# Performance work log

Measured on AMD Instinct MI355X. Metric: run time of the kernel, lower is better.

Reference implementation:

```python
import jax, jax.numpy as jnp
import numpy as np

B = 8192
I = 1024
H = 1024


def _xavier(key, out_dim, in_dim):
    limit = float(np.sqrt(6.0 / (in_dim + out_dim)))
    return jax.random.uniform(key, (out_dim, in_dim), jnp.float32, -limit, limit)


def setup_inputs() -> dict:
    key = jax.random.key(0)
    ks = jax.random.split(key, 16)
    inp = {
        "x": jax.random.normal(ks[0], (B, I), jnp.float32),
        "h_prev": jax.random.normal(ks[1], (B, H), jnp.float32),
        "c_prev": jax.random.normal(ks[2], (B, H), jnp.float32),
        # input->hidden weights (hidden_size, input_size), hidden->hidden (hidden_size, hidden_size)
        "Wxi": _xavier(ks[3], H, I), "Whi": _xavier(ks[4], H, H),
        "Wxf": _xavier(ks[5], H, I), "Whf": _xavier(ks[6], H, H),
        "Wxc": _xavier(ks[7], H, I), "Whc": _xavier(ks[8], H, H),
        "Wxo": _xavier(ks[9], H, I), "Who": _xavier(ks[10], H, H),
        "bxi": jnp.zeros((H,), jnp.float32), "bhi": jnp.zeros((H,), jnp.float32),
        # forget-gate biases initialized to ones per _init_weights
        "bxf": jnp.ones((H,), jnp.float32), "bhf": jnp.ones((H,), jnp.float32),
        "bxc": jnp.zeros((H,), jnp.float32), "bhc": jnp.zeros((H,), jnp.float32),
        "bxo": jnp.zeros((H,), jnp.float32), "bho": jnp.zeros((H,), jnp.float32),
    }
    return inp


def reference(x, h_prev, c_prev,
              Wxi, Whi, Wxf, Whf, Wxc, Whc, Wxo, Who,
              bxi, bhi, bxf, bhf, bxc, bhc, bxo, bho):
    # Fuse the 8 small linears into two GEMMs: stack along the output (gate) axis.
    Wx = jnp.concatenate([Wxi, Wxf, Wxc, Wxo], axis=0)   # (4H, I)
    Wh = jnp.concatenate([Whi, Whf, Whc, Who], axis=0)   # (4H, H)
    bx = jnp.concatenate([bxi, bxf, bxc, bxo], axis=0)    # (4H,)
    bh = jnp.concatenate([bhi, bhf, bhc, bho], axis=0)    # (4H,)
    gates = x @ Wx.T + h_prev @ Wh.T + (bx + bh)           # (B, 4H)
    zi, zf, zc, zo = jnp.split(gates, 4, axis=1)
    i = jax.nn.sigmoid(zi)
    f = jax.nn.sigmoid(zf)
    g = jnp.tanh(zc)
    o = jax.nn.sigmoid(zo)
    c_new = f * c_prev + i * g
    h_new = o * jnp.tanh(c_new)
    return (h_new, c_new)
```

## Files before the change

### kernel.cpp

```cpp
#include <hip/hip_runtime.h>
#include <hip/hip_bf16.h>
#include <stdint.h>


#define B_DIM 8192
#define I_DIM 1024
#define H_DIM 1024
#define K_DIM 2048
#define N_DIM 4096
#define NKT   32

typedef short bf16x8 __attribute__((ext_vector_type(8)));
typedef float f32x4 __attribute__((ext_vector_type(4)));

__device__ __forceinline__ unsigned short f2bf(float f) {
  unsigned int u = __float_as_uint(f);
  u += 0x7FFFu + ((u >> 16) & 1u);
  return (unsigned short)(u >> 16);
}

__global__ void pack_AB_kernel(const float* __restrict__ x, const float* __restrict__ h,
                               const float* __restrict__ Wxi, const float* __restrict__ Whi,
                               const float* __restrict__ Wxf, const float* __restrict__ Whf,
                               const float* __restrict__ Wxc, const float* __restrict__ Whc,
                               const float* __restrict__ Wxo, const float* __restrict__ Who,
                               unsigned short* __restrict__ outA,
                               unsigned short* __restrict__ outB) {
  const int totalA = B_DIM * K_DIM / 8;
  const int total  = totalA + N_DIM * K_DIM / 8;
  for (int idx = blockIdx.x * blockDim.x + threadIdx.x; idx < total;
       idx += gridDim.x * blockDim.x) {
    const float* src;
    unsigned short* dst;
    if (idx < totalA) {
      int row = idx >> 8;
      int col = (idx & 255) * 8;
      src = (col < I_DIM) ? (x + (size_t)row * I_DIM + col)
                          : (h + (size_t)row * H_DIM + (col - I_DIM));
      dst = outA + (size_t)idx * 8;
    } else {
      int u2 = idx - totalA;
      int lane_ = u2 & 63, nn = (u2 >> 6) & 3, kk = (u2 >> 8) & 1;
      int kt = (u2 >> 9) & 31, wn = (u2 >> 14) & 3, bn = u2 >> 16;
      int r = bn * 256 + wn * 64 + nn * 16 + (lane_ & 15);
      int k = kt * 64 + kk * 32 + (lane_ >> 4) * 8;
      int g = (r >> 4) & 3;
      int hh = ((r >> 6) << 4) | (r & 15);
      src = (k < I_DIM)
          ? ((g == 0 ? Wxi : g == 1 ? Wxf : g == 2 ? Wxc : Wxo) + (size_t)hh * I_DIM + k)
          : ((g == 0 ? Whi : g == 1 ? Whf : g == 2 ? Whc : Who) + (size_t)hh * H_DIM + (k - I_DIM));
      dst = outB + (size_t)u2 * 8;
    }
    const float4* s4 = (const float4*)src;
    float4 v0 = s4[0], v1 = s4[1];
    bf16x8 o;
    o[0] = f2bf(v0.x); o[1] = f2bf(v0.y); o[2] = f2bf(v0.z); o[3] = f2bf(v0.w);
    o[4] = f2bf(v1.x); o[5] = f2bf(v1.y); o[6] = f2bf(v1.z); o[7] = f2bf(v1.w);
    *(bf16x8*)dst = o;
  }
}


#define QUAD(MH, KOFF, BR) do {                                               \
    bf16x8 aq[4];                                                             \
    _Pragma("unroll") for (int mf = 0; mf < 4; ++mf)                          \
      aq[mf] = *(const bf16x8*)(ldsAr + _bo + (MH)*8192 + mf * 2048 + (KOFF));\
    __builtin_amdgcn_s_setprio(1);                                            \
    _Pragma("unroll") for (int mf = 0; mf < 4; ++mf)                          \
    _Pragma("unroll") for (int nn = 0; nn < 4; ++nn)                          \
      acc[(MH)*4 + mf][nn] = __builtin_amdgcn_mfma_f32_16x16x32_bf16(         \
          aq[mf], BR[nn], acc[(MH)*4 + mf][nn], 0, 0, 0);                     \
    __builtin_amdgcn_s_setprio(0);                                            \
  } while (0)

#define KTILE(BUF, KT, BC0, BN0) do {                                         \
    const int _bo  = (BUF) * 32768;                                           \
    const int _bo1 = ((BUF) ^ 1) * 32768;                                     \
    int _kt1 = (KT) + 1 < NKT ? (KT) + 1 : NKT - 1;                           \
    const unsigned short* _ga = gAst + (size_t)_kt1 * 64;                     \
    bf16x8 ar0 = *(const bf16x8*)(_ga);                                       \
    bf16x8 ar1 = *(const bf16x8*)(_ga + 8);                                   \
    bf16x8 ar2 = *(const bf16x8*)(_ga + 16);                                  \
    bf16x8 ar3 = *(const bf16x8*)(_ga + 24);                                  \
    _Pragma("unroll") for (int nn = 0; nn < 4; ++nn)                          \
      Bk1[nn] = *(const bf16x8*)(gBfr + (size_t)(KT) * 4096 + 2048 + nn*512); \
    _Pragma("unroll") for (int nn = 0; nn < 4; ++nn)                          \
      BN0[nn] = *(const bf16x8*)(gBfr + (size_t)_kt1 * 4096 + nn * 512);      \
    QUAD(0, rd0, BC0);                                                        \
    QUAD(1, rd0, BC0);                                                        \
    *(bf16x8*)(ldsAw + _bo1 + woff0) = ar0;                                   \
    *(bf16x8*)(ldsAw + _bo1 + woff1) = ar1;                                   \
    QUAD(0, rd1, Bk1);                                                        \
    QUAD(1, rd1, Bk1);                                                        \
    *(bf16x8*)(ldsAw + _bo1 + woff2) = ar2;                                   \
    *(bf16x8*)(ldsAw + _bo1 + woff3) = ar3;                                   \
    __syncthreads();                                                          \
  } while (0)

__launch_bounds__(512, 2)
__global__ void lstm_gemm_kernel(const unsigned short* __restrict__ A,
                                 const unsigned short* __restrict__ Bp,
                                 const float* __restrict__ c_prev,
                                 const float* __restrict__ bxi, const float* __restrict__ bhi,
                                 const float* __restrict__ bxf, const float* __restrict__ bhf,
                                 const float* __restrict__ bxc, const float* __restrict__ bhc,
                                 const float* __restrict__ bxo, const float* __restrict__ bho,
                                 float* __restrict__ out) {
  __shared__ __align__(16) char lds[65536];

  const int nwg = gridDim.x;
  int bid = blockIdx.x;
  int q = nwg >> 3;
  int wg = (bid & 7) * q + (bid >> 3);
  int bm = wg >> 4;
  int bn = wg & 15;

  int tid = threadIdx.x;
  int lane = tid & 63;
  int wid = tid >> 6;
  int wm = wid >> 2;
  int wn = wid & 3;

  const unsigned short* gAst = A + (size_t)(bm * 256 + (tid >> 1)) * K_DIM + (tid & 1) * 32;
  char* ldsAw = lds + (tid >> 1) * 128;
  int wr7 = (tid >> 1) & 7;
  int woff0 = ((((tid & 1) * 4 + 0) ^ wr7) << 4);
  int woff1 = ((((tid & 1) * 4 + 1) ^ wr7) << 4);
  int woff2 = ((((tid & 1) * 4 + 2) ^ wr7) << 4);
  int woff3 = ((((tid & 1) * 4 + 3) ^ wr7) << 4);

  const unsigned short* gBfr = Bp + (size_t)(bn * 4 + wn) * 131072 + lane * 8;

  int c15 = lane & 15;
  int kl = lane >> 4;
  const char* ldsAr = lds + wm * 16384 + c15 * 128;
  int rd0 = ((kl) ^ (lane & 7)) << 4;
  int rd1 = ((4 | kl) ^ (lane & 7)) << 4;

  f32x4 acc[8][4];
  f32x4 zero = {0.f, 0.f, 0.f, 0.f};
#pragma unroll
  for (int m = 0; m < 8; ++m)
#pragma unroll
    for (int n = 0; n < 4; ++n) acc[m][n] = zero;

  bf16x8 Bk0A[4], Bk0B[4], Bk1[4];

#pragma unroll
  for (int nn = 0; nn < 4; ++nn)
    Bk0A[nn] = *(const bf16x8*)(gBfr + nn * 512);
  {
    bf16x8 a0 = *(const bf16x8*)(gAst);
    bf16x8 a1 = *(const bf16x8*)(gAst + 8);
    bf16x8 a2 = *(const bf16x8*)(gAst + 16);
    bf16x8 a3 = *(const bf16x8*)(gAst + 24);
    *(bf16x8*)(ldsAw + woff0) = a0;
    *(bf16x8*)(ldsAw + woff1) = a1;
    *(bf16x8*)(ldsAw + woff2) = a2;
    *(bf16x8*)(ldsAw + woff3) = a3;
  }
  __syncthreads();

#pragma unroll 1
  for (int kt = 0; kt < NKT; kt += 2) {
    KTILE(0, kt, Bk0A, Bk0B);
    KTILE(1, kt + 1, Bk0B, Bk0A);
  }

  int h = (bn * 4 + wn) * 16 + c15;
  float bi = bxi[h] + bhi[h];
  float bf_ = bxf[h] + bhf[h];
  float bc = bxc[h] + bhc[h];
  float bo = bxo[h] + bho[h];
  int row0 = bm * 256 + wm * 128 + kl * 4;
#pragma unroll
  for (int mi = 0; mi < 8; ++mi) {
#pragma unroll
    for (int j = 0; j < 4; ++j) {
      int r = row0 + mi * 16 + j;
      size_t off = (size_t)r * H_DIM + h;
      float zi = acc[mi][0][j] + bi;
      float zf = acc[mi][1][j] + bf_;
      float zc = acc[mi][2][j] + bc;
      float zo = acc[mi][3][j] + bo;
      float ig = 1.f / (1.f + __expf(-zi));
      float fg = 1.f / (1.f + __expf(-zf));
      float e2 = __expf(-2.f * zc);
      float gg = (1.f - e2) / (1.f + e2);
      float og = 1.f / (1.f + __expf(-zo));
      float cp = c_prev[off];
      float cn = fg * cp + ig * gg;
      float e2c = __expf(-2.f * cn);
      float th = (1.f - e2c) / (1.f + e2c);
      out[off] = og * th;
      out[(size_t)B_DIM * H_DIM + off] = cn;
    }
  }
}

extern "C" void kernel_launch(void* const* d_in, const int* in_sizes, int n_in,
                              void* d_out, int out_size, void* d_ws, size_t ws_size,
                              hipStream_t stream) {
  const float* x      = (const float*)d_in[0];
  const float* h_prev = (const float*)d_in[1];
  const float* c_prev = (const float*)d_in[2];
  const float* Wxi = (const float*)d_in[3];
  const float* Whi = (const float*)d_in[4];
  const float* Wxf = (const float*)d_in[5];
  const float* Whf = (const float*)d_in[6];
  const float* Wxc = (const float*)d_in[7];
  const float* Whc = (const float*)d_in[8];
  const float* Wxo = (const float*)d_in[9];
  const float* Who = (const float*)d_in[10];
  const float* bxi = (const float*)d_in[11];
  const float* bhi = (const float*)d_in[12];
  const float* bxf = (const float*)d_in[13];
  const float* bhf = (const float*)d_in[14];
  const float* bxc = (const float*)d_in[15];
  const float* bhc = (const float*)d_in[16];
  const float* bxo = (const float*)d_in[17];
  const float* bho = (const float*)d_in[18];

  unsigned short* Abf = (unsigned short*)d_ws;
  unsigned short* Bbf = (unsigned short*)((char*)d_ws + (size_t)B_DIM * K_DIM * 2);

  pack_AB_kernel<<<2048, 256, 0, stream>>>(x, h_prev,
      Wxi, Whi, Wxf, Whf, Wxc, Whc, Wxo, Who, Abf, Bbf);
  lstm_gemm_kernel<<<512, 512, 0, stream>>>(Abf, Bbf, c_prev,
      bxi, bhi, bxf, bhf, bxc, bhc, bxo, bho, (float*)d_out);
}
```

Measured before the change: 163.8 us.

## Convert activations to bf16 inside GEMM and stage weights via direct-to-LDS loads

Drops the separate pass that packed x and h_prev into bf16 in a workspace. The GEMM now reads fp32 activations directly and converts them while writing to LDS. Weights are packed row-major and staged into LDS with global_load_lds async copies, double-buffered, instead of being read from a fragment-packed layout straight into registers. This removes an extra round trip to global memory for the activation matrix. In exchange, LDS per block doubles to 128KB, which likely breaks the two-blocks-per-CU launch bound, and each block reads twice as many activation bytes.

```diff
diff --git a/kernel.cpp b/kernel.cpp
--- a/kernel.cpp
+++ b/kernel.cpp
@@ -19,47 +19,60 @@
   return (unsigned short)(u >> 16);
 }
 
-__global__ void pack_AB_kernel(const float* __restrict__ x, const float* __restrict__ h,
-                               const float* __restrict__ Wxi, const float* __restrict__ Whi,
-                               const float* __restrict__ Wxf, const float* __restrict__ Whf,
-                               const float* __restrict__ Wxc, const float* __restrict__ Whc,
-                               const float* __restrict__ Wxo, const float* __restrict__ Who,
-                               unsigned short* __restrict__ outA,
-                               unsigned short* __restrict__ outB) {
-  const int totalA = B_DIM * K_DIM / 8;
-  const int total  = totalA + N_DIM * K_DIM / 8;
+__device__ __forceinline__ short f2bf16s(float f) {
+  __hip_bfloat16 t = __float2bfloat16(f);
+  return *reinterpret_cast<short*>(&t);
+}
+
+__device__ __forceinline__ bf16x8 cvt8(float4 a, float4 b) {
+  bf16x8 o;
+  o[0] = f2bf16s(a.x); o[1] = f2bf16s(a.y); o[2] = f2bf16s(a.z); o[3] = f2bf16s(a.w);
+  o[4] = f2bf16s(b.x); o[5] = f2bf16s(b.y); o[6] = f2bf16s(b.z); o[7] = f2bf16s(b.w);
+  return o;
+}
+
+__global__ void pack_B_kernel(const float* __restrict__ Wxi, const float* __restrict__ Whi,
+                              const float* __restrict__ Wxf, const float* __restrict__ Whf,
+                              const float* __restrict__ Wxc, const float* __restrict__ Whc,
+                              const float* __restrict__ Wxo, const float* __restrict__ Who,
+                              unsigned short* __restrict__ outB) {
+  const int total = N_DIM * K_DIM / 8;
   for (int idx = blockIdx.x * blockDim.x + threadIdx.x; idx < total;
        idx += gridDim.x * blockDim.x) {
-    const float* src;
-    unsigned short* dst;
-    if (idx < totalA) {
-      int row = idx >> 8;
-      int col = (idx & 255) * 8;
-      src = (col < I_DIM) ? (x + (size_t)row * I_DIM + col)
-                          : (h + (size_t)row * H_DIM + (col - I_DIM));
-      dst = outA + (size_t)idx * 8;
+    int r = idx >> 8;
+    int k = (idx & 255) * 8;
+    int g = (r >> 4) & 3;
+    int h = ((r >> 6) << 4) | (r & 15);
+    const float* base;
+    if (k < I_DIM) {
+      base = (g == 0) ? Wxi : (g == 1) ? Wxf : (g == 2) ? Wxc : Wxo;
+      base += (size_t)h * I_DIM + k;
     } else {
-      int u2 = idx - totalA;
-      int lane_ = u2 & 63, nn = (u2 >> 6) & 3, kk = (u2 >> 8) & 1;
-      int kt = (u2 >> 9) & 31, wn = (u2 >> 14) & 3, bn = u2 >> 16;
-      int r = bn * 256 + wn * 64 + nn * 16 + (lane_ & 15);
-      int k = kt * 64 + kk * 32 + (lane_ >> 4) * 8;
-      int g = (r >> 4) & 3;
-      int hh = ((r >> 6) << 4) | (r & 15);
-      src = (k < I_DIM)
-          ? ((g == 0 ? Wxi : g == 1 ? Wxf : g == 2 ? Wxc : Wxo) + (size_t)hh * I_DIM + k)
-          : ((g == 0 ? Whi : g == 1 ? Whf : g == 2 ? Whc : Who) + (size_t)hh * H_DIM + (k - I_DIM));
-      dst = outB + (size_t)u2 * 8;
+      base = (g == 0) ? Whi : (g == 1) ? Whf : (g == 2) ? Whc : Who;
+      base += (size_t)h * H_DIM + (k - I_DIM);
     }
-    const float4* s4 = (const float4*)src;
+    const float4* s4 = (const float4*)base;
     float4 v0 = s4[0], v1 = s4[1];
     bf16x8 o;
     o[0] = f2bf(v0.x); o[1] = f2bf(v0.y); o[2] = f2bf(v0.z); o[3] = f2bf(v0.w);
     o[4] = f2bf(v1.x); o[5] = f2bf(v1.y); o[6] = f2bf(v1.z); o[7] = f2bf(v1.w);
-    *(bf16x8*)dst = o;
-  }
-}
-
+    *(bf16x8*)(outB + (size_t)idx * 8) = o;
+  }
+}
+
+
+#define STAGE_B(gptr, slotoff, ktile) do {                                        \
+    int _ktc = (ktile) < NKT ? (ktile) : (NKT - 1);                               \
+    const unsigned short* _g = (gptr) + (size_t)_ktc * 64;                        \
+    __builtin_amdgcn_global_load_lds(                                             \
+        (const __attribute__((address_space(1))) void*)_g,                        \
+        (__attribute__((address_space(3))) void*)(lds + (slotoff) + wid * 1024),  \
+        16, 0, 0);                                                                \
+    __builtin_amdgcn_global_load_lds(                                             \
+        (const __attribute__((address_space(1))) void*)(_g + (size_t)64 * K_DIM), \
+        (__attribute__((address_space(3))) void*)(lds + (slotoff) + 8192 + wid * 1024), \
+        16, 0, 0);                                                                \
+  } while (0)
 
 #define QUAD(MH, KOFF, BR) do {                                               \
     bf16x8 aq[4];                                                             \
@@ -73,32 +86,34 @@
     __builtin_amdgcn_s_setprio(0);                                            \
   } while (0)
 
+#define A_SRC(KTC) ((((KTC) < 16) ? (xg + (size_t)arow * I_DIM + (KTC) * 64)      \
+                                  : (hg + (size_t)arow * H_DIM + ((KTC) - 16) * 64)) + acol)
+
 #define KTILE(BUF, KT, BC0, BN0) do {                                         \
     const int _bo  = (BUF) * 32768;                                           \
     const int _bo1 = ((BUF) ^ 1) * 32768;                                     \
     int _kt1 = (KT) + 1 < NKT ? (KT) + 1 : NKT - 1;                           \
-    const unsigned short* _ga = gAst + (size_t)_kt1 * 64;                     \
-    bf16x8 ar0 = *(const bf16x8*)(_ga);                                       \
-    bf16x8 ar1 = *(const bf16x8*)(_ga + 8);                                   \
-    bf16x8 ar2 = *(const bf16x8*)(_ga + 16);                                  \
-    bf16x8 ar3 = *(const bf16x8*)(_ga + 24);                                  \
+    const float4* _as = (const float4*)A_SRC(_kt1);                           \
+    float4 f0 = _as[0], f1 = _as[1], f2 = _as[2], f3 = _as[3];                \
     _Pragma("unroll") for (int nn = 0; nn < 4; ++nn)                          \
       Bk1[nn] = *(const bf16x8*)(gBfr + (size_t)(KT) * 4096 + 2048 + nn*512); \
     _Pragma("unroll") for (int nn = 0; nn < 4; ++nn)                          \
       BN0[nn] = *(const bf16x8*)(gBfr + (size_t)_kt1 * 4096 + nn * 512);      \
     QUAD(0, rd0, BC0);                                                        \
     QUAD(1, rd0, BC0);                                                        \
-    *(bf16x8*)(ldsAw + _bo1 + woff0) = ar0;                                   \
-    *(bf16x8*)(ldsAw + _bo1 + woff1) = ar1;                                   \
+    *(bf16x8*)(ldsAw + _bo1 + woff0) = cvt8(f0, f1);                          \
+    *(bf16x8*)(ldsAw + _bo1 + woff1) = cvt8(f2, f3);                          \
+    float4 f4 = _as[4], f5 = _as[5], f6 = _as[6], f7 = _as[7];                \
     QUAD(0, rd1, Bk1);                                                        \
     QUAD(1, rd1, Bk1);                                                        \
-    *(bf16x8*)(ldsAw + _bo1 + woff2) = ar2;                                   \
-    *(bf16x8*)(ldsAw + _bo1 + woff3) = ar3;                                   \
+    *(bf16x8*)(ldsAw + _bo1 + woff2) = cvt8(f4, f5);                          \
+    *(bf16x8*)(ldsAw + _bo1 + woff3) = cvt8(f6, f7);                          \
     __syncthreads();                                                          \
   } while (0)
 
 __launch_bounds__(512, 2)
-__global__ void lstm_gemm_kernel(const unsigned short* __restrict__ A,
+__global__ void lstm_gemm_kernel(const float* __restrict__ xg,
+                                 const float* __restrict__ hg,
                                  const unsigned short* __restrict__ Bp,
                                  const float* __restrict__ c_prev,
                                  const float* __restrict__ bxi, const float* __restrict__ bhi,
@@ -106,7 +121,7 @@
                                  const float* __restrict__ bxc, const float* __restrict__ bhc,
                                  const float* __restrict__ bxo, const float* __restrict__ bho,
                                  float* __restrict__ out) {
-  __shared__ __align__(16) char lds[65536];
+  __shared__ __align__(16) char lds[131072];
 
   const int nwg = gridDim.x;
   int bid = blockIdx.x;
@@ -121,7 +136,8 @@
   int wm = wid >> 2;
   int wn = wid & 3;
 
-  const unsigned short* gAst = A + (size_t)(bm * 256 + (tid >> 1)) * K_DIM + (tid & 1) * 32;
+  int arow = bm * 256 + (tid >> 1);
+  int acol = (tid & 1) * 32;
   char* ldsAw = lds + (tid >> 1) * 128;
   int wr7 = (tid >> 1) & 7;
   int woff0 = ((((tid & 1) * 4 + 0) ^ wr7) << 4);
@@ -129,13 +145,18 @@
   int woff2 = ((((tid & 1) * 4 + 2) ^ wr7) << 4);
   int woff3 = ((((tid & 1) * 4 + 3) ^ wr7) << 4);
 
-  const unsigned short* gBfr = Bp + (size_t)(bn * 4 + wn) * 131072 + lane * 8;
+  int srow = lane >> 3;
+  int schunk = (lane & 7) ^ srow;
+  const unsigned short* gB0p = Bp + (size_t)(bn * 256 + wid * 8 + srow) * K_DIM + schunk * 8;
+  const unsigned short* gB1p = gB0p + (size_t)128 * K_DIM;
 
   int c15 = lane & 15;
   int kl = lane >> 4;
   const char* ldsAr = lds + wm * 16384 + c15 * 128;
+  const char* ldsBr = lds + 65536 + (wn >> 1) * 16384 + ((wn & 1) * 64 + c15) * 128;
   int rd0 = ((kl) ^ (lane & 7)) << 4;
   int rd1 = ((4 | kl) ^ (lane & 7)) << 4;
+  (void)ldsBr;
 
   f32x4 acc[8][4];
   f32x4 zero = {0.f, 0.f, 0.f, 0.f};
@@ -146,20 +167,52 @@
 
   bf16x8 Bk0A[4], Bk0B[4], Bk1[4];
 
+  const char* ldsBrd = lds + 65536 + (wn >> 1) * 16384 + ((wn & 1) * 64 + c15) * 128;
+
+#undef KTILE
+#define KTILE(BUF, KT, BC0, BN0) do {                                         \
+    const int _bo  = (BUF) * 32768;                                           \
+    const int _bo1 = ((BUF) ^ 1) * 32768;                                     \
+    int _kt1 = (KT) + 1 < NKT ? (KT) + 1 : NKT - 1;                           \
+    const float4* _as = (const float4*)A_SRC(_kt1);                           \
+    float4 f0 = _as[0], f1 = _as[1], f2 = _as[2], f3 = _as[3];                \
+    _Pragma("unroll") for (int nn = 0; nn < 4; ++nn)                          \
+      Bk1[nn] = *(const bf16x8*)(ldsBrd + _bo + nn * 2048 + rd1);             \
+    _Pragma("unroll") for (int nn = 0; nn < 4; ++nn)                          \
+      BN0[nn] = *(const bf16x8*)(ldsBrd + _bo1 + nn * 2048 + rd0);            \
+    QUAD(0, rd0, BC0);                                                        \
+    QUAD(1, rd0, BC0);                                                        \
+    *(bf16x8*)(ldsAw + _bo1 + woff0) = cvt8(f0, f1);                          \
+    *(bf16x8*)(ldsAw + _bo1 + woff1) = cvt8(f2, f3);                          \
+    STAGE_B(gB0p, 65536 + _bo, (KT) + 2);                                     \
+    float4 f4 = _as[4], f5 = _as[5], f6 = _as[6], f7 = _as[7];                \
+    QUAD(0, rd1, Bk1);                                                        \
+    QUAD(1, rd1, Bk1);                                                        \
+    *(bf16x8*)(ldsAw + _bo1 + woff2) = cvt8(f4, f5);                          \
+    *(bf16x8*)(ldsAw + _bo1 + woff3) = cvt8(f6, f7);                          \
+    STAGE_B(gB1p, 65536 + _bo + 16384, (KT) + 2);                             \
+    asm volatile("s_waitcnt vmcnt(4)" ::: "memory");                          \
+    __syncthreads();                                                          \
+  } while (0)
+
+  STAGE_B(gB0p, 65536, 0);
+  STAGE_B(gB1p, 65536 + 16384, 0);
+  STAGE_B(gB0p, 65536 + 32768, 1);
+  STAGE_B(gB1p, 65536 + 32768 + 16384, 1);
+  {
+    const float4* _as = (const float4*)A_SRC(0);
+    float4 f0 = _as[0], f1 = _as[1], f2 = _as[2], f3 = _as[3];
+    float4 f4 = _as[4], f5 = _as[5], f6 = _as[6], f7 = _as[7];
+    *(bf16x8*)(ldsAw + woff0) = cvt8(f0, f1);
+    *(bf16x8*)(ldsAw + woff1) = cvt8(f2, f3);
+    *(bf16x8*)(ldsAw + woff2) = cvt8(f4, f5);
+    *(bf16x8*)(ldsAw + woff3) = cvt8(f6, f7);
+  }
+  asm volatile("s_waitcnt vmcnt(4)" ::: "memory");
+  __syncthreads();
 #pragma unroll
   for (int nn = 0; nn < 4; ++nn)
-    Bk0A[nn] = *(const bf16x8*)(gBfr + nn * 512);
-  {
-    bf16x8 a0 = *(const bf16x8*)(gAst);
-    bf16x8 a1 = *(const bf16x8*)(gAst + 8);
-    bf16x8 a2 = *(const bf16x8*)(gAst + 16);
-    bf16x8 a3 = *(const bf16x8*)(gAst + 24);
-    *(bf16x8*)(ldsAw + woff0) = a0;
-    *(bf16x8*)(ldsAw + woff1) = a1;
-    *(bf16x8*)(ldsAw + woff2) = a2;
-    *(bf16x8*)(ldsAw + woff3) = a3;
-  }
-  __syncthreads();
+    Bk0A[nn] = *(const bf16x8*)(ldsBrd + nn * 2048 + rd0);
 
 #pragma unroll 1
   for (int kt = 0; kt < NKT; kt += 2) {
@@ -221,11 +274,9 @@
   const float* bxo = (const float*)d_in[17];
   const float* bho = (const float*)d_in[18];
 
-  unsigned short* Abf = (unsigned short*)d_ws;
-  unsigned short* Bbf = (unsigned short*)((char*)d_ws + (size_t)B_DIM * K_DIM * 2);
-
-  pack_AB_kernel<<<2048, 256, 0, stream>>>(x, h_prev,
-      Wxi, Whi, Wxf, Whf, Wxc, Whc, Wxo, Who, Abf, Bbf);
-  lstm_gemm_kernel<<<512, 512, 0, stream>>>(Abf, Bbf, c_prev,
+  unsigned short* Bbf = (unsigned short*)d_ws;
+
+  pack_B_kernel<<<1024, 256, 0, stream>>>(Wxi, Whi, Wxf, Whf, Wxc, Whc, Wxo, Who, Bbf);
+  lstm_gemm_kernel<<<512, 512, 0, stream>>>(x, h_prev, Bbf, c_prev,
       bxi, bhi, bxf, bhf, bxc, bhc, bxo, bho, (float*)d_out);
 }
```

After: 235.0 us. +43.5%, slower.
